# Kernel tuning notes

Measured on AMD Instinct MI355X. Metric: run time of the kernel, lower is better.

## Reference

```python
import jax, jax.numpy as jnp
import numpy as np

N_ITEMS = 30000
N_HOPS = 2
TMP = 0.2
EPS = 1e-12


def _l2norm(x):
    # F.normalize(x, dim=1): x / max(||x||_2, eps)
    n = jnp.sqrt(jnp.sum(x * x, axis=1, keepdims=True))
    return x / jnp.maximum(n, EPS)


def setup_inputs() -> dict:
    key = jax.random.key(0)
    ks = jax.random.split(key, 12)
    n_users, n_entities, n_items, d = 50000, 100000, N_ITEMS, 64
    n_rel, n_fac, n_cls = 16, 4, 8
    n_edges, n_inter = 1000000, 500000
    return {
        'user_emb': jax.random.normal(ks[0], (n_users, d), jnp.float32),
        'entity_emb': jax.random.normal(ks[1], (n_entities, d), jnp.float32),
        'cls_emb': jax.random.normal(ks[2], (n_cls, d), jnp.float32),
        'latent_emb': jax.random.normal(ks[3], (n_fac, d), jnp.float32),
        'relation_emb': jax.random.normal(ks[4], (n_rel, d), jnp.float32),
        'disen_weight_att': jax.random.normal(ks[5], (n_fac, n_rel), jnp.float32),
        'edge_index': jax.random.randint(ks[6], (2, n_edges), 0, n_entities, jnp.int32),
        'edge_type': jax.random.randint(ks[7], (n_edges,), 0, n_rel, jnp.int32),
        'inter_user': jax.random.randint(ks[8], (n_inter,), 0, n_users, jnp.int32),
        'inter_item': jax.random.randint(ks[9], (n_inter,), 0, n_items, jnp.int32),
        'inter_val': jax.random.uniform(ks[10], (n_inter,), jnp.float32),
        'inter_cls': jax.random.randint(ks[11], (n_inter,), 0, n_cls, jnp.int32),
    }


def _cls_aggregate(entity_emb, user_emb, cls_emb, latent_emb, relation_emb,
                   disen_weight_att, edge_index, edge_type,
                   inter_user, inter_item, inter_val, inter_cls,
                   n_users, n_cls):
    n_entities = entity_emb.shape[0]
    item_emb = entity_emb[:N_ITEMS]
    # --- KG aggregate: scatter_mean over head of entity_emb[tail]*rel[edge_type]
    head, tail = edge_index[0], edge_index[1]
    msg = entity_emb[tail] * relation_emb[edge_type]            # [E, d]
    ent_sum = jax.ops.segment_sum(msg, head, num_segments=n_entities)
    cnt = jax.ops.segment_sum(jnp.ones_like(head, jnp.float32), head,
                              num_segments=n_entities)
    entity_agg = ent_sum / jnp.maximum(cnt, 1.0)[:, None]
    # --- user aggregate: sparse interact_mat @ item_emb
    u_msg = inter_val[:, None] * item_emb[inter_item]           # [I, d]
    user_agg = jax.ops.segment_sum(u_msg, inter_user, num_segments=n_users)
    # --- intent attention
    user_disen_att = jax.nn.softmax(user_emb @ latent_emb.T, axis=1)  # [U, F]
    disen_weight = jax.nn.softmax(disen_weight_att, axis=-1) @ relation_emb  # [F, d]
    user_agg = user_disen_att @ disen_weight + user_agg
    # --- class attention: inter_cls_mat[c] @ item_emb for each class
    user_cls_att = jax.nn.softmax(user_emb @ cls_emb.T, axis=1)  # [U, C]
    seg = inter_cls * n_users + inter_user
    user_cls = jax.ops.segment_sum(u_msg, seg, num_segments=n_cls * n_users)
    user_cls = user_cls.reshape(n_cls, n_users, -1)              # [C, U, d]
    user_agg = jnp.einsum('cud,uc->ud', user_cls, user_cls_att) + user_agg
    return entity_agg, user_agg


def _mutual_information(t, temperature):
    nt = _l2norm(t)
    scores = jnp.exp(nt @ nt.T / temperature)
    return -jnp.sum(jnp.log(jnp.diag(scores) / jnp.sum(scores, axis=1)))


def reference(user_emb, entity_emb, cls_emb, latent_emb, relation_emb,
              disen_weight_att, edge_index, edge_type, inter_user,
              inter_item, inter_val, inter_cls):
    n_users = user_emb.shape[0]
    n_cls = cls_emb.shape[0]
    entity_res, user_res = entity_emb, user_emb
    e, u = entity_emb, user_emb
    for _ in range(N_HOPS):
        e, u = _cls_aggregate(e, u, cls_emb, latent_emb, relation_emb,
                              disen_weight_att, edge_index, edge_type,
                              inter_user, inter_item, inter_val, inter_cls,
                              n_users, n_cls)
        e = _l2norm(e)
        u = _l2norm(u)
        entity_res = entity_res + e
        user_res = user_res + u
    cor_loss = _mutual_information(disen_weight_att, TMP)
    return entity_res, user_res, cor_loss
```

## Files before the change

kernel.cpp:

```cpp
#include <hip/hip_runtime.h>
#include <math.h>

typedef unsigned int uint;

constexpr int N_USERS  = 50000;
constexpr int N_ENT    = 100000;
constexpr int D        = 64;
constexpr int N_FAC    = 4;
constexpr int N_CLS    = 8;
constexpr int N_REL    = 16;
constexpr int N_EDGES  = 1000000;
constexpr int N_INTER  = 500000;

constexpr int BSH      = 7;
constexpr int SPB      = 1 << BSH;
constexpr int NBKT_E   = (N_ENT   + SPB - 1) / SPB;
constexpr int NBKT_U   = (N_USERS + SPB - 1) / SPB;
constexpr int CHUNK    = 4096;
constexpr int NB_E     = (N_EDGES + CHUNK - 1) / CHUNK;
constexpr int NB_U     = (N_INTER + CHUNK - 1) / CHUNK;
constexpr int EBUF_CAP = 3072;

constexpr int E_ROWS   = N_ENT + 1;

constexpr int CVT_BLKS = 2047;
constexpr int ATT_BLKS = (N_USERS * 16 + 255) / 256;

static_assert(NB_E <= 256 && NB_U <= 256, "k_final local scan assumes NB <= 256");

typedef _Float16 h2_t __attribute__((ext_vector_type(2)));
union U32H2 { uint u; h2_t h; };

__device__ inline float h_lo(uint v) { U32H2 x; x.u = v; return (float)x.h.x; }
__device__ inline float h_hi(uint v) { U32H2 x; x.u = v; return (float)x.h.y; }
__device__ inline uint packh(float a, float b) {
    auto r = __builtin_amdgcn_cvt_pkrtz(a, b);
    union { decltype(r) h; uint u; } x;
    x.h = r;
    return x.u;
}

__device__ inline int wscan64_incl(int x, int lane) {
#pragma unroll
    for (int off = 1; off < 64; off <<= 1) {
        int v = __shfl_up(x, off, 64);
        if (lane >= off) x += v;
    }
    return x;
}

__device__ inline int block_scan_incl(int x, int* wsum) {
    int lane = threadIdx.x & 63, wv = threadIdx.x >> 6;
#pragma unroll
    for (int off = 1; off < 64; off <<= 1) {
        int v = __shfl_up(x, off, 64);
        if (lane >= off) x += v;
    }
    if (lane == 63) wsum[wv] = x;
    __syncthreads();
    if (wv == 0 && lane < 16) {
        int s = wsum[lane];
#pragma unroll
        for (int off = 1; off < 16; off <<= 1) {
            int v = __shfl_up(s, off, 64);
            if (lane >= off) s += v;
        }
        wsum[lane] = s;
    }
    __syncthreads();
    if (wv > 0) x += wsum[wv - 1];
    return x;
}

__global__ void k_cvt_dw(const float2* __restrict__ in, uint* __restrict__ out,
                         int n_src, int n_out,
                         const float* __restrict__ datt,
                         const float* __restrict__ rel,
                         float* __restrict__ dw,
                         float* __restrict__ loss_out,
                         uint4* __restrict__ relh4,
                         int* __restrict__ totE,
                         int* __restrict__ totU,
                         const float* __restrict__ user_emb,
                         const float* __restrict__ latent,
                         const float* __restrict__ cls,
                         float* __restrict__ att4,
                         float* __restrict__ att8) {
    __shared__ float p[N_FAC][N_REL];
    __shared__ float nrm[N_FAC];
    __shared__ float sc[N_FAC][N_FAC];
    int t = threadIdx.x;
    int b = blockIdx.x;
    if (b < CVT_BLKS) {
        for (int i = b * 256 + t; i < n_out; i += CVT_BLKS * 256) {
            if (i < n_src) {
                float2 v = in[i];
                out[i] = packh(v.x, v.y);
            } else {
                out[i] = 0u;
            }
        }
        return;
    }
    if (b == CVT_BLKS) {
        for (int s = t; s < NBKT_E; s += 256) totE[s] = 0;
        for (int s = t; s < NBKT_U; s += 256) totU[s] = 0;
        for (int s = t; s < N_REL * 8; s += 256) {
            int r = s >> 3, kk = s & 7;
            const float* rp = rel + r * 64 + kk * 8;
            relh4[s] = make_uint4(packh(rp[0], rp[1]), packh(rp[2], rp[3]),
                                  packh(rp[4], rp[5]), packh(rp[6], rp[7]));
        }
        if (t < N_FAC) {
            float m = -1e30f;
            for (int r = 0; r < N_REL; ++r) m = fmaxf(m, datt[t * N_REL + r]);
            float tmp[N_REL]; float s = 0.f;
            for (int r = 0; r < N_REL; ++r) { tmp[r] = expf(datt[t * N_REL + r] - m); s += tmp[r]; }
            for (int r = 0; r < N_REL; ++r) p[t][r] = tmp[r] / s;
            float ss = 0.f;
            for (int r = 0; r < N_REL; ++r) { float v = datt[t * N_REL + r]; ss += v * v; }
            nrm[t] = fmaxf(sqrtf(ss), 1e-12f);
        }
        __syncthreads();
        if (t < D) {
            for (int f = 0; f < N_FAC; ++f) {
                float acc = 0.f;
                for (int r = 0; r < N_REL; ++r) acc += p[f][r] * rel[r * D + t];
                dw[f * D + t] = acc;
            }
        }
        if (t < N_FAC * N_FAC) {
            int i = t >> 2, j = t & 3;
            float s = 0.f;
            for (int r = 0; r < N_REL; ++r) s += datt[i * N_REL + r] * datt[j * N_REL + r];
            s /= nrm[i] * nrm[j];
            sc[i][j] = expf(s * 5.0f);
        }
        __syncthreads();
        if (t == 0) {
            float loss = 0.f;
            for (int i = 0; i < N_FAC; ++i) {
                float rowsum = 0.f;
                for (int j = 0; j < N_FAC; ++j) rowsum += sc[i][j];
                loss += logf(sc[i][i] / rowsum);
            }
            *loss_out = -loss;
        }
        return;
    }
    int gid = (b - CVT_BLKS - 1) * 256 + t;
    int row = gid >> 4;
    int lane = gid & 15;
    if (row >= N_USERS) return;
    float4 uv = ((const float4*)user_emb)[row * 16 + lane];
    float dots[12];
#pragma unroll
    for (int f = 0; f < 4; ++f) {
        float4 lv = ((const float4*)latent)[f * 16 + lane];
        dots[f] = uv.x*lv.x + uv.y*lv.y + uv.z*lv.z + uv.w*lv.w;
    }
#pragma unroll
    for (int c = 0; c < 8; ++c) {
        float4 cv = ((const float4*)cls)[c * 16 + lane];
        dots[4+c] = uv.x*cv.x + uv.y*cv.y + uv.z*cv.z + uv.w*cv.w;
    }
#pragma unroll
    for (int j = 0; j < 12; ++j) {
        float v = dots[j];
#pragma unroll
        for (int m = 1; m < 16; m <<= 1) v += __shfl_xor(v, m, 16);
        dots[j] = v;
    }
    float m4 = fmaxf(fmaxf(dots[0], dots[1]), fmaxf(dots[2], dots[3]));
    float e4v[4]; float s4 = 0.f;
#pragma unroll
    for (int f = 0; f < 4; ++f) { e4v[f] = expf(dots[f] - m4); s4 += e4v[f]; }
    float m8 = dots[4];
#pragma unroll
    for (int c = 1; c < 8; ++c) m8 = fmaxf(m8, dots[4+c]);
    float e8v[8]; float s8 = 0.f;
#pragma unroll
    for (int c = 0; c < 8; ++c) { e8v[c] = expf(dots[4+c] - m8); s8 += e8v[c]; }
    if (lane < 4) {
        float v = e4v[0];
#pragma unroll
        for (int f = 1; f < 4; ++f) if (lane == f) v = e4v[f];
        att4[row * 4 + lane] = v / s4;
    }
    if (lane < 8) {
        float v = e8v[0];
#pragma unroll
        for (int c = 1; c < 8; ++c) if (lane == c) v = e8v[c];
        att8[row * 8 + lane] = v / s8;
    }
}

__global__ void k_sort(const int* __restrict__ headE, const int* __restrict__ tailE,
                       const int* __restrict__ etype,
                       const int* __restrict__ iu, const int* __restrict__ ii,
                       const int* __restrict__ icls, const float* __restrict__ ival,
                       uint2* __restrict__ stagE, int* __restrict__ GE, int* __restrict__ RE,
                       uint2* __restrict__ stagU, int* __restrict__ GU, int* __restrict__ RU,
                       int* __restrict__ totE, int* __restrict__ totU) {
    __shared__ int hist[NBKT_E];
    __shared__ int soff[NBKT_E + 1];
    __shared__ int cursor[NBKT_E];
    __shared__ int wsum[16];
    __shared__ uint2 sorted[CHUNK];
    int bid = blockIdx.x;
    bool isE = bid < NB_E;
    int blk  = isE ? bid : bid - NB_E;
    int n    = isE ? N_EDGES : N_INTER;
    int nbkt = isE ? NBKT_E : NBKT_U;
    int base = blk * CHUNK;
    int end  = min(base + CHUNK, n);
    int cblk = end - base;

    for (int b = threadIdx.x; b < nbkt; b += 256) hist[b] = 0;
    __syncthreads();

    uint2 ent[16]; int ebk[16];
#pragma unroll
    for (int j = 0; j < 16; ++j) {
        int i = base + threadIdx.x + j * 256;
        ebk[j] = -1;
        if (i < end) {
            uint x, y; int b;
            if (isE) {
                int h = headE[i];
                x = (uint)h; y = (uint)((tailE[i] << 4) | etype[i]); b = h >> BSH;
            } else {
                int u = iu[i];
                x = (uint)((u << 15) | ii[i]);
                y = (__float_as_uint(ival[i]) & ~7u) | (uint)icls[i];
                b = u >> BSH;
            }
            ent[j] = make_uint2(x, y); ebk[j] = b;
            atomicAdd(&hist[b], 1);
        }
    }
    __syncthreads();

    int b0 = threadIdx.x * 4;
    int lsum[4]; int mysum = 0;
#pragma unroll
    for (int j = 0; j < 4; ++j) {
        int b = b0 + j;
        int v = (b < nbkt) ? hist[b] : 0;
        lsum[j] = mysum; mysum += v;
    }
    int excl = block_scan_incl(mysum, wsum) - mysum;
#pragma unroll
    for (int j = 0; j < 4; ++j) {
        int b = b0 + j;
        if (b < nbkt) soff[b] = excl + lsum[j];
    }
    if (threadIdx.x == 0) soff[nbkt] = cblk;
    __syncthreads();
    for (int b = threadIdx.x; b < nbkt; b += 256) cursor[b] = soff[b];
    __syncthreads();

#pragma unroll
    for (int j = 0; j < 16; ++j) {
        if (ebk[j] >= 0) {
            int p = atomicAdd(&cursor[ebk[j]], 1);
            sorted[p] = ent[j];
        }
    }
    __syncthreads();

    uint2* stag = isE ? stagE : stagU;
    int* G = isE ? GE : GU;
    int* R = isE ? RE : RU;
    int* tot = isE ? totE : totU;
    for (int i = threadIdx.x; i < cblk; i += 256) stag[blk * CHUNK + i] = sorted[i];
    for (int b = threadIdx.x; b < nbkt; b += 256) {
        G[blk * nbkt + b] = hist[b];
        if (hist[b]) atomicAdd(&tot[b], hist[b]);
    }
    for (int b = threadIdx.x; b <= nbkt; b += 256) R[blk * (nbkt + 1) + b] = soff[b];
}

__device__ inline void scan_tot(const int* __restrict__ tot, int* __restrict__ base,
                                int nbkt, int l, int* __restrict__ off_last, int nseg) {
    int carry = 0;
    for (int b = 0; b < nbkt; b += 64) {
        int x = (b + l < nbkt) ? tot[b + l] : 0;
        int incl = wscan64_incl(x, l);
        if (b + l < nbkt) base[b + l] = carry + incl - x;
        carry += __shfl(incl, 63, 64);
    }
    if (l == 0) {
        base[nbkt] = carry;
        off_last[nseg] = carry;
        off_last[nseg + 1] = carry;
    }
}

__global__ void k_base(const int* __restrict__ totE, int* __restrict__ baseE,
                       const int* __restrict__ totU, int* __restrict__ baseU,
                       int* __restrict__ eoff, int* __restrict__ uoff) {
    int t = threadIdx.x;
    if (t < 64) scan_tot(totE, baseE, NBKT_E, t, eoff, N_ENT);
    else        scan_tot(totU, baseU, NBKT_U, t - 64, uoff, N_USERS);
}

__global__ void k_final(const uint2* __restrict__ stagE, const int* __restrict__ GE,
                        const int* __restrict__ RE, const int* __restrict__ baseE,
                        const uint2* __restrict__ stagU, const int* __restrict__ GU,
                        const int* __restrict__ RU, const int* __restrict__ baseU,
                        int* __restrict__ eoff, int* __restrict__ uoff,
                        int* __restrict__ epay, int2* __restrict__ ipv) {
    __shared__ uint2 ebuf[EBUF_CAP];
    __shared__ int cnt[SPB], soff[SPB], cur[SPB];
    __shared__ int wsum[16];
    int bid = blockIdx.x;
    bool isE = bid < NBKT_E;
    int bkt = bid < NBKT_E ? bid : bid - NBKT_E;
    const uint2* stag = isE ? stagE : stagU;
    const int* G  = isE ? GE : GU;
    const int* R  = isE ? RE : RU;
    const int* bb = isE ? baseE : baseU;
    int* off      = isE ? eoff : uoff;
    int NB   = isE ? NB_E : NB_U;
    int nbkt = isE ? NBKT_E : NBKT_U;
    int nseg = isE ? N_ENT : N_USERS;
    int r0 = bb[bkt], r1 = bb[bkt + 1];
    int bsz = r1 - r0;
    int t = threadIdx.x;
    int myc = (t < NB) ? G[t * nbkt + bkt] : 0;
    int mydst = block_scan_incl(myc, wsum) - myc;
    if (t < SPB) cnt[t] = 0;
    if (t < NB) {
        int rs  = R[t * (nbkt + 1) + bkt];
        int re  = R[t * (nbkt + 1) + bkt + 1];
        for (int j = rs; j < re; ++j) {
            int d = mydst + (j - rs);
            if (d < EBUF_CAP) ebuf[d] = stag[t * CHUNK + j];
        }
    }
    __syncthreads();
    for (int i = t; i < bsz; i += 256) {
        uint2 e = ebuf[i];
        int s = (int)(isE ? e.x : (e.x >> 15)) & (SPB - 1);
        atomicAdd(&cnt[s], 1);
    }
    __syncthreads();
    if (t < 64) {
        int a0 = cnt[2 * t], a1 = cnt[2 * t + 1];
        int incl = wscan64_incl(a0 + a1, t);
        int excl = incl - (a0 + a1);
        soff[2 * t] = excl;
        soff[2 * t + 1] = excl + a0;
    }
    __syncthreads();
    if (t < SPB) {
        cur[t] = soff[t];
        int seg = bkt * SPB + t;
        if (seg < nseg) off[seg] = r0 + soff[t];
    }
    __syncthreads();
    for (int i = t; i < bsz; i += 256) {
        uint2 e = ebuf[i];
        int s = (int)(isE ? e.x : (e.x >> 15)) & (SPB - 1);
        int pos = r0 + atomicAdd(&cur[s], 1);
        if (isE) {
            epay[pos] = (int)e.y;
        } else {
            int item = (int)(e.x & 0x7FFF), cls = (int)(e.y & 7u);
            ipv[pos] = make_int2((item << 3) | cls, (int)(e.y & ~7u));
        }
    }
}

template<int MODE>
__global__ __launch_bounds__(256)
void k_hop(const uint4* __restrict__ etab,
           const float4* __restrict__ entbase,
           const float4* __restrict__ usrbase,
           const uint4* __restrict__ ustate_in,
           const uint4* __restrict__ relh4,
           const int* __restrict__ eoff,
           const int* __restrict__ epay,
           const int* __restrict__ uoff,
           const int2* __restrict__ ipv,
           const float4* __restrict__ latent4,
           const float4* __restrict__ cls4,
           const float4* __restrict__ dw4,
           float* __restrict__ att4,
           float* __restrict__ att8,
           uint4* __restrict__ stateE_out,
           uint4* __restrict__ stateU_out,
           float4* __restrict__ outE,
           float4* __restrict__ outU) {
    __shared__ uint4  s_rel[N_REL * 8];
    __shared__ float4 s_dw [N_FAC * 16];
    __shared__ float4 s_lat[N_FAC * 16];
    __shared__ float4 s_cls[N_CLS * 16];
    {
        int t = threadIdx.x;
        if (t < N_REL * 8) s_rel[t] = relh4[t];
        if (t < N_FAC * 16) s_dw[t] = dw4[t];
        if (MODE == 0) {
            if (t < N_FAC * 16) s_lat[t] = latent4[t];
            if (t < N_CLS * 16) s_cls[t] = cls4[t];
        }
    }
    __syncthreads();

    int gid = blockIdx.x * 256 + threadIdx.x;
    int gw = gid >> 3;
    int k = threadIdx.x & 7;
    if (gw >= E_ROWS + N_USERS) return;
    bool isEnt = gw < E_ROWS;
    float a0 = 0.f, a1 = 0.f, a2 = 0.f, a3 = 0.f;
    float a4 = 0.f, a5 = 0.f, a6 = 0.f, a7 = 0.f;

    if (isEnt) {
        int w = gw;
        int beg = eoff[w], end = eoff[w + 1];
        int nE = end - beg;
        const int* pp = epay + beg;
        int pc[8];
#pragma unroll
        for (int q = 0; q < 8; ++q) pc[q] = pp[q];
        for (int bse = 0; bse < nE; bse += 8) {
            int c = nE - bse;
            int pn[8];
#pragma unroll
            for (int q = 0; q < 8; ++q) pn[q] = pp[bse + 8 + q];
            uint4 ev[8], rl[8];
#pragma unroll
            for (int q = 0; q < 8; ++q) {
                int p = (q < c) ? pc[q] : (N_ENT << 4);
                ev[q] = etab[(((size_t)(p >> 4)) << 3) + k];
                rl[q] = s_rel[((p & 15) << 3) + k];
            }
#pragma unroll
            for (int q = 0; q < 8; ++q) {
                a0 = fmaf(h_lo(ev[q].x), h_lo(rl[q].x), a0);
                a1 = fmaf(h_hi(ev[q].x), h_hi(rl[q].x), a1);
                a2 = fmaf(h_lo(ev[q].y), h_lo(rl[q].y), a2);
                a3 = fmaf(h_hi(ev[q].y), h_hi(rl[q].y), a3);
                a4 = fmaf(h_lo(ev[q].z), h_lo(rl[q].z), a4);
                a5 = fmaf(h_hi(ev[q].z), h_hi(rl[q].z), a5);
                a6 = fmaf(h_lo(ev[q].w), h_lo(rl[q].w), a6);
                a7 = fmaf(h_hi(ev[q].w), h_hi(rl[q].w), a7);
            }
#pragma unroll
            for (int q = 0; q < 8; ++q) pc[q] = pn[q];
        }
        float ss = a0*a0 + a1*a1 + a2*a2 + a3*a3 + a4*a4 + a5*a5 + a6*a6 + a7*a7;
#pragma unroll
        for (int m = 1; m < 8; m <<= 1) ss += __shfl_xor(ss, m, 8);
        float s = 1.0f / fmaxf(sqrtf(ss), 1e-12f);
        float v0 = a0*s, v1 = a1*s, v2 = a2*s, v3 = a3*s;
        float v4 = a4*s, v5 = a5*s, v6 = a6*s, v7 = a7*s;
        if (MODE == 0) {
            stateE_out[((size_t)w << 3) + k] =
                make_uint4(packh(v0, v1), packh(v2, v3), packh(v4, v5), packh(v6, v7));
        } else if (w < N_ENT) {
            size_t b = ((size_t)w << 4) + (k << 1);
            float4 b0 = entbase[b], b1 = entbase[b + 1];
            uint4 own = etab[((size_t)w << 3) + k];
            float4 o0 = make_float4(b0.x + h_lo(own.x) + v0, b0.y + h_hi(own.x) + v1,
                                    b0.z + h_lo(own.y) + v2, b0.w + h_hi(own.y) + v3);
            float4 o1 = make_float4(b1.x + h_lo(own.z) + v4, b1.y + h_hi(own.z) + v5,
                                    b1.z + h_lo(own.w) + v6, b1.w + h_hi(own.w) + v7);
            outE[b] = o0; outE[b + 1] = o1;
        }
    } else {
        int w = gw - E_ROWS;
        int beg = uoff[w], end = uoff[w + 1];
        int nE = end - beg;
        const int2* pv = ipv + beg;
        float a8v = att8[w * 8 + k];

        int2 ec[8];
#pragma unroll
        for (int q = 0; q < 8; ++q) ec[q] = pv[q];
        for (int bse = 0; bse < nE; bse += 8) {
            int c = nE - bse;
            int2 en[8];
#pragma unroll
            for (int q = 0; q < 8; ++q) en[q] = pv[bse + 8 + q];
            uint4 ev[8]; float wg[8];
#pragma unroll
            for (int q = 0; q < 8; ++q) {
                int p = ec[q].x;
                int pe = (q < c) ? p : 0;
                ev[q] = etab[(((size_t)(pe >> 3)) << 3) + k];
                float wgt = __int_as_float(ec[q].y) * (1.0f + __shfl(a8v, p & 7, 8));
                wg[q] = (q < c) ? wgt : 0.0f;
            }
#pragma unroll
            for (int q = 0; q < 8; ++q) {
                a0 = fmaf(h_lo(ev[q].x), wg[q], a0);
                a1 = fmaf(h_hi(ev[q].x), wg[q], a1);
                a2 = fmaf(h_lo(ev[q].y), wg[q], a2);
                a3 = fmaf(h_hi(ev[q].y), wg[q], a3);
                a4 = fmaf(h_lo(ev[q].z), wg[q], a4);
                a5 = fmaf(h_hi(ev[q].z), wg[q], a5);
                a6 = fmaf(h_lo(ev[q].w), wg[q], a6);
                a7 = fmaf(h_hi(ev[q].w), wg[q], a7);
            }
#pragma unroll
            for (int q = 0; q < 8; ++q) ec[q] = en[q];
        }
#pragma unroll
        for (int f = 0; f < 4; ++f) {
            float a = att4[w * 4 + f];
            const float4* dd = s_dw + f * 16 + (k << 1);
            float4 d0 = dd[0], d1 = dd[1];
            a0 = fmaf(a, d0.x, a0); a1 = fmaf(a, d0.y, a1);
            a2 = fmaf(a, d0.z, a2); a3 = fmaf(a, d0.w, a3);
            a4 = fmaf(a, d1.x, a4); a5 = fmaf(a, d1.y, a5);
            a6 = fmaf(a, d1.z, a6); a7 = fmaf(a, d1.w, a7);
        }
        float ss = a0*a0 + a1*a1 + a2*a2 + a3*a3 + a4*a4 + a5*a5 + a6*a6 + a7*a7;
#pragma unroll
        for (int m = 1; m < 8; m <<= 1) ss += __shfl_xor(ss, m, 8);
        float s = 1.0f / fmaxf(sqrtf(ss), 1e-12f);
        float v0 = a0*s, v1 = a1*s, v2 = a2*s, v3 = a3*s;
        float v4 = a4*s, v5 = a5*s, v6 = a6*s, v7 = a7*s;
        if (MODE == 0) {
            stateU_out[((size_t)w << 3) + k] =
                make_uint4(packh(v0, v1), packh(v2, v3), packh(v4, v5), packh(v6, v7));
            float d[12];
#pragma unroll
            for (int f = 0; f < 12; ++f) {
                const float4* lp = (f < 4 ? s_lat + f * 16 : s_cls + (f - 4) * 16) + (k << 1);
                float4 l0 = lp[0], l1 = lp[1];
                d[f] = v0*l0.x + v1*l0.y + v2*l0.z + v3*l0.w
                     + v4*l1.x + v5*l1.y + v6*l1.z + v7*l1.w;
            }
#pragma unroll
            for (int j = 0; j < 12; ++j) {
#pragma unroll
                for (int off = 1; off < 8; off <<= 1) d[j] += __shfl_xor(d[j], off, 8);
            }
            float m4 = fmaxf(fmaxf(d[0], d[1]), fmaxf(d[2], d[3]));
            float e40 = expf(d[0] - m4), e41 = expf(d[1] - m4);
            float e42 = expf(d[2] - m4), e43 = expf(d[3] - m4);
            float r4 = 1.0f / (e40 + e41 + e42 + e43);
            if (k < 4) {
                float v = (k == 0) ? e40 : (k == 1) ? e41 : (k == 2) ? e42 : e43;
                att4[w * 4 + k] = v * r4;
            }
            float m8 = d[4];
#pragma unroll
            for (int c = 1; c < 8; ++c) m8 = fmaxf(m8, d[4 + c]);
            float e8[8]; float s8 = 0.f;
#pragma unroll
            for (int c = 0; c < 8; ++c) { e8[c] = expf(d[4 + c] - m8); s8 += e8[c]; }
            float a8e = e8[0];
#pragma unroll
            for (int c = 1; c < 8; ++c) if (k == c) a8e = e8[c];
            att8[w * 8 + k] = a8e / s8;
        } else {
            uint4 own = ustate_in[((size_t)w << 3) + k];
            size_t b = ((size_t)w << 4) + (k << 1);
            float4 b0 = usrbase[b], b1 = usrbase[b + 1];
            float4 o0 = make_float4(b0.x + h_lo(own.x) + v0, b0.y + h_hi(own.x) + v1,
                                    b0.z + h_lo(own.y) + v2, b0.w + h_hi(own.y) + v3);
            float4 o1 = make_float4(b1.x + h_lo(own.z) + v4, b1.y + h_hi(own.z) + v5,
                                    b1.z + h_lo(own.w) + v6, b1.w + h_hi(own.w) + v7);
            outU[b] = o0; outU[b + 1] = o1;
        }
    }
}

extern "C" void kernel_launch(void* const* d_in, const int* in_sizes, int n_in,
                              void* d_out, int out_size, void* d_ws, size_t ws_size,
                              hipStream_t stream) {
    const float* user_emb   = (const float*)d_in[0];
    const float* entity_emb = (const float*)d_in[1];
    const float* cls_emb    = (const float*)d_in[2];
    const float* latent_emb = (const float*)d_in[3];
    const float* rel_emb    = (const float*)d_in[4];
    const float* disen      = (const float*)d_in[5];
    const int*   edge_index = (const int*)d_in[6];
    const int*   edge_type  = (const int*)d_in[7];
    const int*   inter_user = (const int*)d_in[8];
    const int*   inter_item = (const int*)d_in[9];
    const float* inter_val  = (const float*)d_in[10];
    const int*   inter_cls  = (const int*)d_in[11];

    float* out      = (float*)d_out;
    float* out_ent  = out;
    float* out_user = out + (size_t)N_ENT * D;
    float* out_loss = out + (size_t)N_ENT * D + (size_t)N_USERS * D;

    char* w = (char*)d_ws;
    auto alloc = [&](size_t bytes) -> char* {
        char* p = w;
        w += (bytes + 255) & ~(size_t)255;
        return p;
    };
    uint*  ebuf0 = (uint*)alloc((size_t)E_ROWS * 32 * 4);
    uint*  eA    = (uint*)alloc((size_t)E_ROWS * 32 * 4);
    uint*  uA    = (uint*)alloc((size_t)N_USERS * 32 * 4);
    int*   epay  = (int*)alloc((size_t)(N_EDGES + 32) * 4);
    int2*  ipv   = (int2*)alloc((size_t)(N_INTER + 32) * 8);
    int*   eoff  = (int*)alloc((size_t)(N_ENT + 4) * 4);
    int*   uoff  = (int*)alloc((size_t)(N_USERS + 4) * 4);
    int*   GE    = (int*)alloc((size_t)NB_E * NBKT_E * 4);
    int*   RE    = (int*)alloc((size_t)NB_E * (NBKT_E + 1) * 4);
    int*   GU    = (int*)alloc((size_t)NB_U * NBKT_U * 4);
    int*   RU    = (int*)alloc((size_t)NB_U * (NBKT_U + 1) * 4);
    int*   totE  = (int*)alloc((size_t)NBKT_E * 4);
    int*   totU  = (int*)alloc((size_t)NBKT_U * 4);
    int*   baseE = (int*)alloc((size_t)(NBKT_E + 1) * 4);
    int*   baseU = (int*)alloc((size_t)(NBKT_U + 1) * 4);
    uint4* relh  = (uint4*)alloc((size_t)N_REL * 8 * 16);
    float* dw    = (float*)alloc((size_t)N_FAC * D * 4);
    float* att4  = (float*)alloc((size_t)N_USERS * N_FAC * 4);
    float* att8  = (float*)alloc((size_t)N_USERS * N_CLS * 4);

    uint2* stagE = (uint2*)eA;
    uint2* stagU = (uint2*)uA;

    const int* head = edge_index;
    const int* tail = edge_index + N_EDGES;

    k_cvt_dw<<<CVT_BLKS + 1 + ATT_BLKS, 256, 0, stream>>>(
        (const float2*)entity_emb, ebuf0, N_ENT * 32, E_ROWS * 32,
        disen, rel_emb, dw, out_loss, relh, totE, totU,
        user_emb, latent_emb, cls_emb, att4, att8);
    k_sort <<<NB_E + NB_U, 256, 0, stream>>>(head, tail, edge_type,
                                             inter_user, inter_item, inter_cls, inter_val,
                                             stagE, GE, RE, stagU, GU, RU, totE, totU);
    k_base <<<1, 128, 0, stream>>>(totE, baseE, totU, baseU, eoff, uoff);
    k_final<<<NBKT_E + NBKT_U, 256, 0, stream>>>(stagE, GE, RE, baseE,
                                                 stagU, GU, RU, baseU,
                                                 eoff, uoff, epay, ipv);

    const int hop_blocks = ((E_ROWS + N_USERS) * 8 + 255) / 256;

    k_hop<0><<<hop_blocks, 256, 0, stream>>>((const uint4*)ebuf0, nullptr,
                                             (const float4*)user_emb, nullptr,
                                             relh, eoff, epay, uoff, ipv,
                                             (const float4*)latent_emb,
                                             (const float4*)cls_emb,
                                             (const float4*)dw,
                                             att4, att8,
                                             (uint4*)eA, (uint4*)uA,
                                             nullptr, nullptr);

    k_hop<1><<<hop_blocks, 256, 0, stream>>>((const uint4*)eA,
                                             (const float4*)entity_emb,
                                             (const float4*)user_emb,
                                             (const uint4*)uA,
                                             relh, eoff, epay, uoff, ipv,
                                             (const float4*)latent_emb,
                                             (const float4*)cls_emb,
                                             (const float4*)dw,
                                             att4, att8,
                                             nullptr, nullptr,
                                             (float4*)out_ent, (float4*)out_user);
}
```

Measured before the change: 136.4 us.

## Store gathered entity embeddings as FP8 to halve gather bandwidth

Entity embedding tables read by the edge and interaction gathers are now stored as packed FP8 (8 bytes per 8 values) instead of FP16. The conversion kernel and the first hop write FP8 copies, and the second hop keeps a separate FP16 copy for its own-row residual term. The goal is to roughly halve the random-gather memory traffic in both hops, which dominates the runtime. The cost is a large precision loss, since FP8 has about a 3-bit mantissa, and an extra state write in hop 0, so accuracy tolerances may be violated.

```diff
diff --git a/kernel.cpp b/kernel.cpp
--- a/kernel.cpp
+++ b/kernel.cpp
@@ -29,6 +29,7 @@
 static_assert(NB_E <= 256 && NB_U <= 256, "k_final local scan assumes NB <= 256");
 
 typedef _Float16 h2_t __attribute__((ext_vector_type(2)));
+typedef float f32x2 __attribute__((ext_vector_type(2)));
 union U32H2 { uint u; h2_t h; };
 
 __device__ inline float h_lo(uint v) { U32H2 x; x.u = v; return (float)x.h.x; }
@@ -40,6 +41,15 @@
     return x.u;
 }
 
+template<bool HI>
+__device__ inline f32x2 f8_unpk(uint v) {
+    return __builtin_amdgcn_cvt_pk_f32_fp8((int)v, HI);
+}
+template<bool HI>
+__device__ inline uint f8_pk(float a, float b, uint old) {
+    return (uint)__builtin_amdgcn_cvt_pk_fp8_f32(a, b, (int)old, HI);
+}
+
 __device__ inline int wscan64_incl(int x, int lane) {
 #pragma unroll
     for (int off = 1; off < 64; off <<= 1) {
@@ -72,8 +82,8 @@
     return x;
 }
 
-__global__ void k_cvt_dw(const float2* __restrict__ in, uint* __restrict__ out,
-                         int n_src, int n_out,
+__global__ void k_cvt_dw(const float* __restrict__ ent_emb,
+                         uint2* __restrict__ out8,
                          const float* __restrict__ datt,
                          const float* __restrict__ rel,
                          float* __restrict__ dw,
@@ -92,13 +102,18 @@
     int t = threadIdx.x;
     int b = blockIdx.x;
     if (b < CVT_BLKS) {
-        for (int i = b * 256 + t; i < n_out; i += CVT_BLKS * 256) {
-            if (i < n_src) {
-                float2 v = in[i];
-                out[i] = packh(v.x, v.y);
-            } else {
-                out[i] = 0u;
-            }
+        for (int i = b * 256 + t; i < E_ROWS * 8; i += CVT_BLKS * 256) {
+            int row = i >> 3, kk = i & 7;
+            uint2 o = make_uint2(0u, 0u);
+            if (row < N_ENT) {
+                const float4* rp = (const float4*)ent_emb + row * 16 + kk * 2;
+                float4 A = rp[0], B = rp[1];
+                uint lo = 0, hi = 0;
+                lo = f8_pk<false>(A.x, A.y, lo); lo = f8_pk<true>(A.z, A.w, lo);
+                hi = f8_pk<false>(B.x, B.y, hi); hi = f8_pk<true>(B.z, B.w, hi);
+                o = make_uint2(lo, hi);
+            }
+            out8[i] = o;
         }
         return;
     }
@@ -375,7 +390,8 @@
 
 template<int MODE>
 __global__ __launch_bounds__(256)
-void k_hop(const uint4* __restrict__ etab,
+void k_hop(const uint2* __restrict__ etab8,
+           const uint4* __restrict__ ownE16,
            const float4* __restrict__ entbase,
            const float4* __restrict__ usrbase,
            const uint4* __restrict__ ustate_in,
@@ -389,7 +405,8 @@
            const float4* __restrict__ dw4,
            float* __restrict__ att4,
            float* __restrict__ att8,
-           uint4* __restrict__ stateE_out,
+           uint2* __restrict__ stateE8_out,
+           uint4* __restrict__ stateE16_out,
            uint4* __restrict__ stateU_out,
            float4* __restrict__ outE,
            float4* __restrict__ outU) {
@@ -429,23 +446,25 @@
             int pn[8];
 #pragma unroll
             for (int q = 0; q < 8; ++q) pn[q] = pp[bse + 8 + q];
-            uint4 ev[8], rl[8];
+            uint2 ev[8]; uint4 rl[8];
 #pragma unroll
             for (int q = 0; q < 8; ++q) {
                 int p = (q < c) ? pc[q] : (N_ENT << 4);
-                ev[q] = etab[(((size_t)(p >> 4)) << 3) + k];
+                ev[q] = etab8[(((size_t)(p >> 4)) << 3) + k];
                 rl[q] = s_rel[((p & 15) << 3) + k];
             }
 #pragma unroll
             for (int q = 0; q < 8; ++q) {
-                a0 = fmaf(h_lo(ev[q].x), h_lo(rl[q].x), a0);
-                a1 = fmaf(h_hi(ev[q].x), h_hi(rl[q].x), a1);
-                a2 = fmaf(h_lo(ev[q].y), h_lo(rl[q].y), a2);
-                a3 = fmaf(h_hi(ev[q].y), h_hi(rl[q].y), a3);
-                a4 = fmaf(h_lo(ev[q].z), h_lo(rl[q].z), a4);
-                a5 = fmaf(h_hi(ev[q].z), h_hi(rl[q].z), a5);
-                a6 = fmaf(h_lo(ev[q].w), h_lo(rl[q].w), a6);
-                a7 = fmaf(h_hi(ev[q].w), h_hi(rl[q].w), a7);
+                f32x2 x0 = f8_unpk<false>(ev[q].x), x1 = f8_unpk<true>(ev[q].x);
+                f32x2 x2 = f8_unpk<false>(ev[q].y), x3 = f8_unpk<true>(ev[q].y);
+                a0 = fmaf(x0.x, h_lo(rl[q].x), a0);
+                a1 = fmaf(x0.y, h_hi(rl[q].x), a1);
+                a2 = fmaf(x1.x, h_lo(rl[q].y), a2);
+                a3 = fmaf(x1.y, h_hi(rl[q].y), a3);
+                a4 = fmaf(x2.x, h_lo(rl[q].z), a4);
+                a5 = fmaf(x2.y, h_hi(rl[q].z), a5);
+                a6 = fmaf(x3.x, h_lo(rl[q].w), a6);
+                a7 = fmaf(x3.y, h_hi(rl[q].w), a7);
             }
 #pragma unroll
             for (int q = 0; q < 8; ++q) pc[q] = pn[q];
@@ -457,12 +476,16 @@
         float v0 = a0*s, v1 = a1*s, v2 = a2*s, v3 = a3*s;
         float v4 = a4*s, v5 = a5*s, v6 = a6*s, v7 = a7*s;
         if (MODE == 0) {
-            stateE_out[((size_t)w << 3) + k] =
+            uint lo = 0, hi = 0;
+            lo = f8_pk<false>(v0, v1, lo); lo = f8_pk<true>(v2, v3, lo);
+            hi = f8_pk<false>(v4, v5, hi); hi = f8_pk<true>(v6, v7, hi);
+            stateE8_out[((size_t)w << 3) + k] = make_uint2(lo, hi);
+            stateE16_out[((size_t)w << 3) + k] =
                 make_uint4(packh(v0, v1), packh(v2, v3), packh(v4, v5), packh(v6, v7));
         } else if (w < N_ENT) {
             size_t b = ((size_t)w << 4) + (k << 1);
             float4 b0 = entbase[b], b1 = entbase[b + 1];
-            uint4 own = etab[((size_t)w << 3) + k];
+            uint4 own = ownE16[((size_t)w << 3) + k];
             float4 o0 = make_float4(b0.x + h_lo(own.x) + v0, b0.y + h_hi(own.x) + v1,
                                     b0.z + h_lo(own.y) + v2, b0.w + h_hi(own.y) + v3);
             float4 o1 = make_float4(b1.x + h_lo(own.z) + v4, b1.y + h_hi(own.z) + v5,
@@ -484,25 +507,27 @@
             int2 en[8];
 #pragma unroll
             for (int q = 0; q < 8; ++q) en[q] = pv[bse + 8 + q];
-            uint4 ev[8]; float wg[8];
+            uint2 ev[8]; float wg[8];
 #pragma unroll
             for (int q = 0; q < 8; ++q) {
                 int p = ec[q].x;
                 int pe = (q < c) ? p : 0;
-                ev[q] = etab[(((size_t)(pe >> 3)) << 3) + k];
+                ev[q] = etab8[(((size_t)(pe >> 3)) << 3) + k];
                 float wgt = __int_as_float(ec[q].y) * (1.0f + __shfl(a8v, p & 7, 8));
                 wg[q] = (q < c) ? wgt : 0.0f;
             }
 #pragma unroll
             for (int q = 0; q < 8; ++q) {
-                a0 = fmaf(h_lo(ev[q].x), wg[q], a0);
-                a1 = fmaf(h_hi(ev[q].x), wg[q], a1);
-                a2 = fmaf(h_lo(ev[q].y), wg[q], a2);
-                a3 = fmaf(h_hi(ev[q].y), wg[q], a3);
-                a4 = fmaf(h_lo(ev[q].z), wg[q], a4);
-                a5 = fmaf(h_hi(ev[q].z), wg[q], a5);
-                a6 = fmaf(h_lo(ev[q].w), wg[q], a6);
-                a7 = fmaf(h_hi(ev[q].w), wg[q], a7);
+                f32x2 x0 = f8_unpk<false>(ev[q].x), x1 = f8_unpk<true>(ev[q].x);
+                f32x2 x2 = f8_unpk<false>(ev[q].y), x3 = f8_unpk<true>(ev[q].y);
+                a0 = fmaf(x0.x, wg[q], a0);
+                a1 = fmaf(x0.y, wg[q], a1);
+                a2 = fmaf(x1.x, wg[q], a2);
+                a3 = fmaf(x1.y, wg[q], a3);
+                a4 = fmaf(x2.x, wg[q], a4);
+                a5 = fmaf(x2.y, wg[q], a5);
+                a6 = fmaf(x3.x, wg[q], a6);
+                a7 = fmaf(x3.y, wg[q], a7);
             }
 #pragma unroll
             for (int q = 0; q < 8; ++q) ec[q] = en[q];
@@ -597,9 +622,10 @@
         w += (bytes + 255) & ~(size_t)255;
         return p;
     };
-    uint*  ebuf0 = (uint*)alloc((size_t)E_ROWS * 32 * 4);
-    uint*  eA    = (uint*)alloc((size_t)E_ROWS * 32 * 4);
-    uint*  uA    = (uint*)alloc((size_t)N_USERS * 32 * 4);
+    uint2* etab8 = (uint2*)alloc((size_t)E_ROWS * 8 * 8);
+    uint2* eA8   = (uint2*)alloc((size_t)E_ROWS * 8 * 8);
+    uint4* eA16  = (uint4*)alloc((size_t)E_ROWS * 8 * 16);
+    uint4* uA16  = (uint4*)alloc((size_t)N_USERS * 8 * 16);
     int*   epay  = (int*)alloc((size_t)(N_EDGES + 32) * 4);
     int2*  ipv   = (int2*)alloc((size_t)(N_INTER + 32) * 8);
     int*   eoff  = (int*)alloc((size_t)(N_ENT + 4) * 4);
@@ -617,14 +643,14 @@
     float* att4  = (float*)alloc((size_t)N_USERS * N_FAC * 4);
     float* att8  = (float*)alloc((size_t)N_USERS * N_CLS * 4);
 
-    uint2* stagE = (uint2*)eA;
-    uint2* stagU = (uint2*)uA;
+    uint2* stagE = (uint2*)eA16;
+    uint2* stagU = (uint2*)uA16;
 
     const int* head = edge_index;
     const int* tail = edge_index + N_EDGES;
 
     k_cvt_dw<<<CVT_BLKS + 1 + ATT_BLKS, 256, 0, stream>>>(
-        (const float2*)entity_emb, ebuf0, N_ENT * 32, E_ROWS * 32,
+        entity_emb, etab8,
         disen, rel_emb, dw, out_loss, relh, totE, totU,
         user_emb, latent_emb, cls_emb, att4, att8);
     k_sort <<<NB_E + NB_U, 256, 0, stream>>>(head, tail, edge_type,
@@ -637,25 +663,25 @@
 
     const int hop_blocks = ((E_ROWS + N_USERS) * 8 + 255) / 256;
 
-    k_hop<0><<<hop_blocks, 256, 0, stream>>>((const uint4*)ebuf0, nullptr,
+    k_hop<0><<<hop_blocks, 256, 0, stream>>>(etab8, nullptr, nullptr,
                                              (const float4*)user_emb, nullptr,
                                              relh, eoff, epay, uoff, ipv,
                                              (const float4*)latent_emb,
                                              (const float4*)cls_emb,
                                              (const float4*)dw,
                                              att4, att8,
-                                             (uint4*)eA, (uint4*)uA,
+                                             eA8, eA16, uA16,
                                              nullptr, nullptr);
 
-    k_hop<1><<<hop_blocks, 256, 0, stream>>>((const uint4*)eA,
+    k_hop<1><<<hop_blocks, 256, 0, stream>>>(eA8, (const uint4*)eA16,
                                              (const float4*)entity_emb,
                                              (const float4*)user_emb,
-                                             (const uint4*)uA,
+                                             (const uint4*)uA16,
                                              relh, eoff, epay, uoff, ipv,
                                              (const float4*)latent_emb,
                                              (const float4*)cls_emb,
                                              (const float4*)dw,
                                              att4, att8,
-                                             nullptr, nullptr,
+                                             nullptr, nullptr, nullptr,
                                              (float4*)out_ent, (float4*)out_user);
 }
```

Result: no change. 135.6 us (-0.6%).
